# Kernel tuning notes

Measured on AMD Instinct MI355X. Metric: run time of the kernel, lower is better.

The kernel has to match this reference:

```python
import jax, jax.numpy as jnp
import numpy as np

D_MODEL = 1024
NHEADS = 16
E_HEAD = D_MODEL // NHEADS  # 64
ROPE_BASE = 10000.0


def _rope_cos_sin(L, dim, base, dtype):
    # dim = E_head (even); inv_freq over pairs, GPT-NeoX half-split convention
    inv_freq = 1.0 / (base ** (jnp.arange(0, dim, 2, dtype=jnp.float32) / dim))
    pos = jnp.arange(L, dtype=jnp.float32)
    freqs = pos[:, None] * inv_freq[None, :]  # [L, dim/2]
    return jnp.cos(freqs).astype(dtype), jnp.sin(freqs).astype(dtype)


def _apply_rope(t, cos, sin):
    # t: [B, H, L, Dh]; rotate-half formulation
    d2 = t.shape[-1] // 2
    t1, t2 = t[..., :d2], t[..., d2:]
    return jnp.concatenate([t1 * cos - t2 * sin, t1 * sin + t2 * cos], axis=-1)


def setup_inputs() -> dict:
    key = jax.random.key(0)
    ks = jax.random.split(key, 5)
    B, L = 4, 2048
    x = jax.random.normal(ks[0], (B, L, D_MODEL), dtype=jnp.float32)
    s_in = 1.0 / np.sqrt(D_MODEL)
    W_packed = jax.random.normal(ks[1], (3 * D_MODEL, D_MODEL), dtype=jnp.float32) * s_in
    b_packed = jax.random.normal(ks[2], (3 * D_MODEL,), dtype=jnp.float32) * 0.02
    W_out = jax.random.normal(ks[3], (D_MODEL, D_MODEL), dtype=jnp.float32) * s_in
    b_out = jax.random.normal(ks[4], (D_MODEL,), dtype=jnp.float32) * 0.02
    return {"x": x, "W_packed": W_packed, "b_packed": b_packed, "W_out": W_out, "b_out": b_out}


def reference(x, W_packed, b_packed, W_out, b_out):
    B, L, _ = x.shape
    # 1) packed QKV projection (query is key is value path)
    qkv = jnp.einsum('ble,fe->blf', x, W_packed) + b_packed  # [B, L, 3*D]
    q, k, v = jnp.split(qkv, 3, axis=-1)
    # 2) split heads -> [B, H, L, Dh]
    def heads(t):
        return t.reshape(B, L, NHEADS, E_HEAD).transpose(0, 2, 1, 3)
    q, k, v = heads(q), heads(k), heads(v)
    # 3) RoPE on q, k
    cos, sin = _rope_cos_sin(L, E_HEAD, ROPE_BASE, x.dtype)
    q = _apply_rope(q, cos, sin)
    k = _apply_rope(k, cos, sin)
    # 4) SDPA (non-causal, no dropout)
    scale = 1.0 / np.sqrt(E_HEAD)
    scores = jnp.einsum('bhqd,bhkd->bhqk', q, k) * scale
    attn = jax.nn.softmax(scores, axis=-1)
    out = jnp.einsum('bhqk,bhkd->bhqd', attn, v)
    # 5) merge heads + output projection
    out = out.transpose(0, 2, 1, 3).reshape(B, L, D_MODEL)
    return jnp.einsum('bld,ed->ble', out, W_out) + b_out
```

## Files before the change

### kernel.cpp

```cpp
#include <hip/hip_runtime.h>
#include <hip/hip_bf16.h>
#include <stdint.h>

#define L_SEQ 2048
#define NB    4
#define NH    16
#define EH    64
#define DM    1024
#define MTOT  (NB * L_SEQ)

typedef __attribute__((ext_vector_type(8))) short bf16x8;
typedef __attribute__((ext_vector_type(4))) float f32x4;
typedef __attribute__((ext_vector_type(16))) float f32x16;

static __device__ __forceinline__ float bf2f(short u) {
    union { unsigned int i; float f; } c;
    c.i = ((unsigned int)(unsigned short)u) << 16;
    return c.f;
}
static __device__ __forceinline__ short f2bf(float f) {
    union { float f; unsigned int i; } c; c.f = f;
    unsigned int x = c.i;
    unsigned int r = (x + 0x7fffu + ((x >> 16) & 1u)) >> 16;
    return (short)(unsigned short)r;
}
static __device__ __forceinline__ unsigned cvtpk(float lo, float hi) {
    unsigned r;
    asm volatile("v_cvt_pk_bf16_f32 %0, %1, %2" : "=v"(r) : "v"(lo), "v"(hi));
    return r;
}

static __device__ __forceinline__ void gload_lds16(const void* g, void* lds) {
    __builtin_amdgcn_global_load_lds(
        (const __attribute__((address_space(1))) unsigned int*)g,
        (__attribute__((address_space(3))) unsigned int*)lds, 16, 0, 0);
}

__global__ __launch_bounds__(256) void cvt3_k(const float* __restrict__ x,
                                              const float* __restrict__ wp,
                                              const float* __restrict__ wo,
                                              short* __restrict__ xb,
                                              short* __restrict__ wpb,
                                              short* __restrict__ wob,
                                              float* __restrict__ tab) {
    int bid = blockIdx.x;
    if (bid >= 12288) {
        int i = (bid - 12288) * 256 + threadIdx.x;
        int l = i >> 5, d = i & 31;
        float inv = powf(10000.0f, -(float)d * (1.0f / 32.0f));
        float fr = (float)l * inv;
        tab[i]         = cosf(fr);
        tab[65536 + i] = sinf(fr);
        return;
    }
    const float* src; short* dst; int i;
    if (bid < 8192)       { src = x;  dst = xb;  i = bid * 256 + threadIdx.x; }
    else if (bid < 11264) { src = wp; dst = wpb; i = (bid - 8192) * 256 + threadIdx.x; }
    else                  { src = wo; dst = wob; i = (bid - 11264) * 256 + threadIdx.x; }
    float4 v = ((const float4*)src)[i];
    short4 o;
    o.x = f2bf(v.x); o.y = f2bf(v.y); o.z = f2bf(v.z); o.w = f2bf(v.w);
    ((short4*)dst)[i] = o;
}

template<int OUTBF16, int NBN, int NCOL>
__global__ __launch_bounds__(512, 2) void gemmA_k(const short* __restrict__ A,
                                                  const short* __restrict__ Bt,
                                                  const float* __restrict__ bias,
                                                  void* __restrict__ Cv) {
    __shared__ short lds[2][384 * 32];
    const int t = threadIdx.x;
    const int w = t >> 6, l = t & 63;
    const int wm = w >> 1, wn = w & 1;
    const int lr = l & 15, lh = l >> 4;

    const int nblk = NBN * 32;
    int fid = blockIdx.x + blockIdx.y * NBN;
    int swz = (fid & 7) * (nblk >> 3) + (fid >> 3);
    const int n0 = (swz % NBN) * 128;
    const int m0 = (swz / NBN) * 256;

    const int lrow = l >> 2;
    const int schunk = (l & 3) ^ ((l >> 3) & 3);

    const short* Ag = A + (size_t)(m0 + lrow) * 1024 + schunk * 8;
    const short* Bg = Bt + (size_t)(n0 + lrow) * 1024 + schunk * 8;

    auto STAGE = [&](int kt, int buf) {
        gload_lds16(Ag + (size_t)(w * 32) * 1024 + kt * 32,      &lds[buf][(w * 32) * 32]);
        gload_lds16(Ag + (size_t)(w * 32 + 16) * 1024 + kt * 32, &lds[buf][(w * 32 + 16) * 32]);
        gload_lds16(Bg + (size_t)(w * 16) * 1024 + kt * 32,      &lds[buf][8192 + (w * 16) * 32]);
    };

    f32x4 acc[4][4] = {};

    STAGE(0, 0);
    STAGE(1, 1);
    asm volatile("s_waitcnt vmcnt(3)" ::: "memory");
    __builtin_amdgcn_s_barrier();

    const int fch = (lh ^ ((lr >> 1) & 3)) << 3;

#pragma unroll 2
    for (int kt = 0; kt < 32; ++kt) {
        const int c = kt & 1;
        const short* Al = &lds[c][0];
        const short* Bl = &lds[c][8192];

        bf16x8 bfr[4], af[4];
#pragma unroll
        for (int nj = 0; nj < 4; ++nj)
            bfr[nj] = *(const bf16x8*)(Bl + (wn * 64 + nj * 16 + lr) * 32 + fch);
#pragma unroll
        for (int mi = 0; mi < 4; ++mi)
            af[mi] = *(const bf16x8*)(Al + (wm * 64 + mi * 16 + lr) * 32 + fch);

        __builtin_amdgcn_s_setprio(1);
#pragma unroll
        for (int mi = 0; mi < 4; ++mi)
#pragma unroll
            for (int nj = 0; nj < 4; ++nj)
                acc[mi][nj] = __builtin_amdgcn_mfma_f32_16x16x32_bf16(
                    af[mi], bfr[nj], acc[mi][nj], 0, 0, 0);
        __builtin_amdgcn_s_setprio(0);

        asm volatile("s_waitcnt lgkmcnt(0)" ::: "memory");
        __builtin_amdgcn_s_barrier();
        if (kt + 2 < 32) {
            STAGE(kt + 2, c);
            asm volatile("s_waitcnt vmcnt(3)" ::: "memory");
        } else {
            asm volatile("s_waitcnt vmcnt(0)" ::: "memory");
        }
        __builtin_amdgcn_s_barrier();
    }

#pragma unroll
    for (int mi = 0; mi < 4; ++mi) {
#pragma unroll
        for (int nj = 0; nj < 4; ++nj) {
            const int row = m0 + wm * 64 + mi * 16 + lh * 4;
            const int col = n0 + wn * 64 + nj * 16 + lr;
            const float bsv = bias[col];
#pragma unroll
            for (int j = 0; j < 4; ++j) {
                float v = acc[mi][nj][j] + bsv;
                if (OUTBF16)
                    ((short*)Cv)[(size_t)(row + j) * NCOL + col] = f2bf(v);
                else
                    ((float*)Cv)[(size_t)(row + j) * NCOL + col] = v;
            }
        }
    }
}

__global__ __launch_bounds__(256) void gemm_out_k(const short* __restrict__ A,
                                                  const short* __restrict__ Bt,
                                                  const float* __restrict__ bias,
                                                  float* __restrict__ Cv,
                                                  int N, int K) {
    __shared__ short As[128 * 64];
    __shared__ short Bs[128 * 64];
    const int t = threadIdx.x;
    const int w = t >> 6, l = t & 63;
    const int wr = w >> 1, wc = w & 1;
    const int lr = l & 15, lh = l >> 4;
    const int m0 = blockIdx.y * 128, n0 = blockIdx.x * 128;
    const int srow = t >> 3;
    const int scol = (t & 7) * 8;

    f32x4 acc[4][4] = {};

    const short* Ab = A + (size_t)(m0 + srow) * K + scol;
    const short* Bb = Bt + (size_t)(n0 + srow) * K + scol;

    for (int k0 = 0; k0 < K; k0 += 64) {
        __syncthreads();
#pragma unroll
        for (int i = 0; i < 4; i++) {
            gload_lds16(Ab + (size_t)(i * 32) * K + k0, As + i * 2048 + w * 512);
            gload_lds16(Bb + (size_t)(i * 32) * K + k0, Bs + i * 2048 + w * 512);
        }
        __syncthreads();
#pragma unroll
        for (int kk = 0; kk < 2; kk++) {
            bf16x8 af[4], bfr[4];
#pragma unroll
            for (int mi = 0; mi < 4; mi++)
                af[mi] = *(const bf16x8*)(As + (wr * 64 + mi * 16 + lr) * 64 + kk * 32 + lh * 8);
#pragma unroll
            for (int nj = 0; nj < 4; nj++)
                bfr[nj] = *(const bf16x8*)(Bs + (wc * 64 + nj * 16 + lr) * 64 + kk * 32 + lh * 8);
            __builtin_amdgcn_s_setprio(1);
#pragma unroll
            for (int mi = 0; mi < 4; mi++)
#pragma unroll
                for (int nj = 0; nj < 4; nj++)
                    acc[mi][nj] = __builtin_amdgcn_mfma_f32_16x16x32_bf16(
                        af[mi], bfr[nj], acc[mi][nj], 0, 0, 0);
            __builtin_amdgcn_s_setprio(0);
        }
    }
#pragma unroll
    for (int mi = 0; mi < 4; mi++) {
#pragma unroll
        for (int nj = 0; nj < 4; nj++) {
            const int row = m0 + wr * 64 + mi * 16 + lh * 4;
            const int col = n0 + wc * 64 + nj * 16 + lr;
            const float bsv = bias[col];
#pragma unroll
            for (int j = 0; j < 4; j++)
                Cv[(size_t)(row + j) * N + col] = acc[mi][nj][j] + bsv;
        }
    }
}

__global__ __launch_bounds__(256) void scatter_k(const short* __restrict__ qkv,
                                                 const float* __restrict__ tab,
                                                 short* __restrict__ Kd,
                                                 short* __restrict__ Vt) {
    int bid = blockIdx.x;
    if (bid < 4096) {
        int idx = bid * 256 + threadIdx.x;
        int dp = (idx & 7) * 4;
        int h = (idx >> 3) & 15;
        int bl = idx >> 7;
        int l = bl & (L_SEQ - 1);
        int b = bl >> 11;
        float4 cs = *(const float4*)&tab[l * 32 + dp];
        float4 sn = *(const float4*)&tab[65536 + l * 32 + dp];
        const short* row = qkv + (size_t)bl * 3072;
        short4 k1 = *(const short4*)&row[1024 + h * 64 + dp];
        short4 k2 = *(const short4*)&row[1024 + h * 64 + dp + 32];
        size_t ob = ((size_t)((b * 16 + h) * 2048 + l)) * 64;
        union { unsigned u[2]; short4 s4; } e1, e2;
        e1.u[0] = cvtpk(bf2f(k1.x) * cs.x - bf2f(k2.x) * sn.x,
                        bf2f(k1.y) * cs.y - bf2f(k2.y) * sn.y);
        e1.u[1] = cvtpk(bf2f(k1.z) * cs.z - bf2f(k2.z) * sn.z,
                        bf2f(k1.w) * cs.w - bf2f(k2.w) * sn.w);
        e2.u[0] = cvtpk(bf2f(k1.x) * sn.x + bf2f(k2.x) * cs.x,
                        bf2f(k1.y) * sn.y + bf2f(k2.y) * cs.y);
        e2.u[1] = cvtpk(bf2f(k1.z) * sn.z + bf2f(k2.z) * cs.z,
                        bf2f(k1.w) * sn.w + bf2f(k2.w) * cs.w);
        int r7 = l & 7;
        int c1 = ((dp >> 3) ^ r7) * 8 + (dp & 7);
        int c2 = (((dp >> 3) | 4) ^ r7) * 8 + (dp & 7);
        *(short4*)(Kd + ob + c1) = e1.s4;
        *(short4*)(Kd + ob + c2) = e2.s4;
        return;
    }
    __shared__ short tile[64 * 65];
    int bid2 = bid - 4096;
    int l0 = (bid2 & 31) * 64;
    int bh = bid2 >> 5;
    int t = threadIdx.x;
    int b = bh >> 4, h = bh & 15;
#pragma unroll
    for (int i = 0; i < 16; i++) {
        int l = i * 4 + (t >> 6);
        int d = t & 63;
        tile[d * 65 + l] = qkv[(size_t)(b * 2048 + l0 + l) * 3072 + 2048 + h * 64 + d];
    }
    __syncthreads();
#pragma unroll
    for (int i = 0; i < 16; i++) {
        int d = i * 4 + (t >> 6);
        int lx = t & 63;
        int cl = (lx & ~0xC) | ((lx & 4) << 1) | ((lx & 8) >> 1);
        int lp = l0 | ((((cl >> 3) ^ (d & 7)) << 3)) | (cl & 7);
        Vt[(size_t)(bh * 64 + d) * 2048 + lp] = tile[d * 65 + lx];
    }
}

__global__ __launch_bounds__(512, 2) void attn_k(const short* __restrict__ qkv,
                                                 const short* __restrict__ Kg,
                                                 const short* __restrict__ Vt,
                                                 const float* __restrict__ tab,
                                                 short* __restrict__ O) {
    __shared__ short Ks[3][64 * 64];
    __shared__ short Vs[3][64 * 64];
    const int t = threadIdx.x;
    const int w = t >> 6, l = t & 63;
    const int q = l & 31, hi = l >> 5;
    const int r7 = l & 7;

    const int od = blockIdx.x + blockIdx.y * 8;
    const int qblk = (od >> 3) & 7;
    const int bh = (od & 7) * 8 + (od >> 6);
    const int q0 = qblk * 256;
    const int b = bh >> 4, h = bh & 15;

    const short* Kb = Kg + (size_t)bh * (2048 * 64);
    const short* Vb = Vt + (size_t)bh * (64 * 2048);

    const int qrow = q0 + w * 32 + q;

    const short* Qsrc = qkv + (size_t)(b * 2048 + qrow) * 3072 + h * 64;
    bf16x8 qraw[4];
#pragma unroll
    for (int ds = 0; ds < 4; ds++)
        qraw[ds] = *(const bf16x8*)(Qsrc + ds * 16 + hi * 8);
    const float sc = 0.18033688011112042f;
    bf16x8 qf[4];
#pragma unroll
    for (int dsL = 0; dsL < 2; dsL++) {
        bf16x8 r1 = qraw[dsL], r2 = qraw[dsL + 2];
        union { unsigned u[4]; bf16x8 v; } lo, hg;
#pragma unroll
        for (int p = 0; p < 4; p++) {
            float2 c2 = *(const float2*)&tab[qrow * 32 + dsL * 16 + hi * 8 + 2 * p];
            float2 s2 = *(const float2*)&tab[65536 + qrow * 32 + dsL * 16 + hi * 8 + 2 * p];
            float a0 = bf2f(r1[2 * p]),     b0 = bf2f(r2[2 * p]);
            float a1 = bf2f(r1[2 * p + 1]), b1 = bf2f(r2[2 * p + 1]);
            lo.u[p] = cvtpk((a0 * c2.x - b0 * s2.x) * sc, (a1 * c2.y - b1 * s2.y) * sc);
            hg.u[p] = cvtpk((a0 * s2.x + b0 * c2.x) * sc, (a1 * s2.y + b1 * c2.y) * sc);
        }
        qf[dsL] = lo.v; qf[dsL + 2] = hg.v;
    }

    const short one_bf = (short)0x3F80;
    const bf16x8 ones = {one_bf, one_bf, one_bf, one_bf, one_bf, one_bf, one_bf, one_bf};

    f32x16 o0 = {}, o1 = {}, os = {};

    const int grow = w * 8 + (l >> 3);
    const int gcol = r7 * 8;

    gload_lds16(Kb + (size_t)grow * 64 + gcol,        &Ks[0][w * 512]);
    gload_lds16(Vb + (size_t)grow * 2048 + gcol,      &Vs[0][w * 512]);
    gload_lds16(Kb + (size_t)(64 + grow) * 64 + gcol, &Ks[1][w * 512]);
    gload_lds16(Vb + (size_t)grow * 2048 + 64 + gcol, &Vs[1][w * 512]);
    asm volatile("s_waitcnt vmcnt(2)" ::: "memory");
    __builtin_amdgcn_s_barrier();

    const short* Kc = &Ks[0][0];  const short* Vc = &Vs[0][0];
    const short* Kn = &Ks[1][0];  const short* Vn = &Vs[1][0];
    short*       Kf = &Ks[2][0];  short*       Vf = &Vs[2][0];

    for (int it = 0; it < 32; ++it) {
        if (it < 30) {
            const int kn = (it + 2) * 64;
            gload_lds16(Kb + (size_t)(kn + grow) * 64 + gcol, Kf + w * 512);
            gload_lds16(Vb + (size_t)grow * 2048 + kn + gcol, Vf + w * 512);
        }

        f32x16 s0 = {}, s1 = {};
#pragma unroll
        for (int ds = 0; ds < 4; ds++) {
            const int ch = ((ds << 1) | hi) ^ r7;
            bf16x8 k0f = *(const bf16x8*)(Kc + q * 64 + ch * 8);
            bf16x8 k1f = *(const bf16x8*)(Kc + (32 + q) * 64 + ch * 8);
            __builtin_amdgcn_s_setprio(1);
            s0 = __builtin_amdgcn_mfma_f32_32x32x16_bf16(k0f, qf[ds], s0, 0, 0, 0);
            s1 = __builtin_amdgcn_mfma_f32_32x32x16_bf16(k1f, qf[ds], s1, 0, 0, 0);
            __builtin_amdgcn_s_setprio(0);
        }

#pragma unroll
        for (int r = 0; r < 16; r++) {
            s0[r] = __builtin_amdgcn_exp2f(s0[r]);
            s1[r] = __builtin_amdgcn_exp2f(s1[r]);
        }

        bf16x8 pf[4];
        {
            union { unsigned u[4]; bf16x8 v; } f;
            f.u[0] = cvtpk(s0[0], s0[1]);  f.u[1] = cvtpk(s0[2], s0[3]);
            f.u[2] = cvtpk(s0[4], s0[5]);  f.u[3] = cvtpk(s0[6], s0[7]);
            pf[0] = f.v;
            f.u[0] = cvtpk(s0[8], s0[9]);  f.u[1] = cvtpk(s0[10], s0[11]);
            f.u[2] = cvtpk(s0[12], s0[13]); f.u[3] = cvtpk(s0[14], s0[15]);
            pf[1] = f.v;
            f.u[0] = cvtpk(s1[0], s1[1]);  f.u[1] = cvtpk(s1[2], s1[3]);
            f.u[2] = cvtpk(s1[4], s1[5]);  f.u[3] = cvtpk(s1[6], s1[7]);
            pf[2] = f.v;
            f.u[0] = cvtpk(s1[8], s1[9]);  f.u[1] = cvtpk(s1[10], s1[11]);
            f.u[2] = cvtpk(s1[12], s1[13]); f.u[3] = cvtpk(s1[14], s1[15]);
            pf[3] = f.v;
        }

#pragma unroll
        for (int ks = 0; ks < 4; ks++) {
            const int ch = ((ks << 1) | hi) ^ r7;
            bf16x8 v0f = *(const bf16x8*)(Vc + q * 64 + ch * 8);
            bf16x8 v1f = *(const bf16x8*)(Vc + (32 + q) * 64 + ch * 8);
            __builtin_amdgcn_s_setprio(1);
            o0 = __builtin_amdgcn_mfma_f32_32x32x16_bf16(v0f, pf[ks], o0, 0, 0, 0);
            o1 = __builtin_amdgcn_mfma_f32_32x32x16_bf16(v1f, pf[ks], o1, 0, 0, 0);
            os = __builtin_amdgcn_mfma_f32_32x32x16_bf16(ones, pf[ks], os, 0, 0, 0);
            __builtin_amdgcn_s_setprio(0);
        }

        asm volatile("s_waitcnt lgkmcnt(0)" ::: "memory");
        if (it < 30) asm volatile("s_waitcnt vmcnt(2)" ::: "memory");
        else         asm volatile("s_waitcnt vmcnt(0)" ::: "memory");
        __builtin_amdgcn_s_barrier();

        const short* tk = Kc; Kc = Kn; Kn = Kf; Kf = (short*)tk;
        const short* tv = Vc; Vc = Vn; Vn = Vf; Vf = (short*)tv;
    }

    const float inv = 1.0f / os[0];
    short* Orow = O + (size_t)(b * 2048 + qrow) * 1024 + h * 64;
#pragma unroll
    for (int g = 0; g < 4; g++) {
        unsigned w0 = cvtpk(o0[g * 4 + 0] * inv, o0[g * 4 + 1] * inv);
        unsigned w1 = cvtpk(o0[g * 4 + 2] * inv, o0[g * 4 + 3] * inv);
        unsigned long long p0 = (unsigned long long)w0 | ((unsigned long long)w1 << 32);
        *(unsigned long long*)(Orow + g * 8 + hi * 4) = p0;
        unsigned w2 = cvtpk(o1[g * 4 + 0] * inv, o1[g * 4 + 1] * inv);
        unsigned w3 = cvtpk(o1[g * 4 + 2] * inv, o1[g * 4 + 3] * inv);
        unsigned long long p1 = (unsigned long long)w2 | ((unsigned long long)w3 << 32);
        *(unsigned long long*)(Orow + 32 + g * 8 + hi * 4) = p1;
    }
}

extern "C" void kernel_launch(void* const* d_in, const int* in_sizes, int n_in,
                              void* d_out, int out_size, void* d_ws, size_t ws_size,
                              hipStream_t stream) {
    const float* x  = (const float*)d_in[0];
    const float* Wp = (const float*)d_in[1];
    const float* bp = (const float*)d_in[2];
    const float* Wo = (const float*)d_in[3];
    const float* bo = (const float*)d_in[4];

    char* ws = (char*)d_ws;
    const size_t SZ_XB  = (size_t)MTOT * DM * 2;
    const size_t SZ_WPB = (size_t)3 * DM * DM * 2;
    const size_t SZ_WOB = (size_t)DM * DM * 2;
    const size_t SZ_QKV = (size_t)MTOT * 3 * DM * 2;
    const size_t SZ_BHLE = (size_t)MTOT * DM * 2;

    short* xb   = (short*)(ws);
    short* wpb  = (short*)(ws + SZ_XB);
    short* wob  = (short*)(ws + SZ_XB + SZ_WPB);
    short* qkvb = (short*)(ws + SZ_XB + SZ_WPB + SZ_WOB);
    short* Kb   = (short*)(ws + SZ_XB + SZ_WPB + SZ_WOB + SZ_QKV);
    short* Vtb  = (short*)(ws + SZ_XB + SZ_WPB + SZ_WOB + SZ_QKV + SZ_BHLE);
    short* Ob   = (short*)(ws + SZ_XB + SZ_WPB + SZ_WOB + SZ_QKV + 2 * SZ_BHLE);
    float* tab  = (float*)(ws + SZ_XB + SZ_WPB + SZ_WOB + SZ_QKV + 3 * SZ_BHLE);

    cvt3_k<<<12544, 256, 0, stream>>>(x, Wp, Wo, xb, wpb, wob, tab);

    gemmA_k<1, 24, 3072><<<dim3(24, 32), 512, 0, stream>>>(xb, wpb, bp, qkvb);

    scatter_k<<<6144, 256, 0, stream>>>(qkvb, tab, Kb, Vtb);

    attn_k<<<dim3(8, 64), 512, 0, stream>>>(qkvb, Kb, Vtb, tab, Ob);

    gemm_out_k<<<dim3(8, 64), 256, 0, stream>>>(Ob, wob, bo, (float*)d_out, DM, DM);
}
```

Baseline: 198.9 us.

## Precompute scaled RoPE Q in scatter kernel; reuse gemmA for output projection

Moves the RoPE rotation and softmax scaling of Q from the attention kernel into the scatter kernel, which now writes a contiguous per-head Q buffer. The attention prologue becomes plain vector loads instead of strided qkv reads plus table lookups. The separate 256-thread output GEMM is dropped and the templated 512-thread gemmA kernel is reused with fp32 output (128x... tiles, 8x32 grid). This costs an extra Q write and read through global memory, and the output GEMM grid shrinks from 512 to 256 blocks.

```diff
diff --git a/kernel.cpp b/kernel.cpp
--- a/kernel.cpp
+++ b/kernel.cpp
@@ -154,69 +154,9 @@
     }
 }
 
-__global__ __launch_bounds__(256) void gemm_out_k(const short* __restrict__ A,
-                                                  const short* __restrict__ Bt,
-                                                  const float* __restrict__ bias,
-                                                  float* __restrict__ Cv,
-                                                  int N, int K) {
-    __shared__ short As[128 * 64];
-    __shared__ short Bs[128 * 64];
-    const int t = threadIdx.x;
-    const int w = t >> 6, l = t & 63;
-    const int wr = w >> 1, wc = w & 1;
-    const int lr = l & 15, lh = l >> 4;
-    const int m0 = blockIdx.y * 128, n0 = blockIdx.x * 128;
-    const int srow = t >> 3;
-    const int scol = (t & 7) * 8;
-
-    f32x4 acc[4][4] = {};
-
-    const short* Ab = A + (size_t)(m0 + srow) * K + scol;
-    const short* Bb = Bt + (size_t)(n0 + srow) * K + scol;
-
-    for (int k0 = 0; k0 < K; k0 += 64) {
-        __syncthreads();
-#pragma unroll
-        for (int i = 0; i < 4; i++) {
-            gload_lds16(Ab + (size_t)(i * 32) * K + k0, As + i * 2048 + w * 512);
-            gload_lds16(Bb + (size_t)(i * 32) * K + k0, Bs + i * 2048 + w * 512);
-        }
-        __syncthreads();
-#pragma unroll
-        for (int kk = 0; kk < 2; kk++) {
-            bf16x8 af[4], bfr[4];
-#pragma unroll
-            for (int mi = 0; mi < 4; mi++)
-                af[mi] = *(const bf16x8*)(As + (wr * 64 + mi * 16 + lr) * 64 + kk * 32 + lh * 8);
-#pragma unroll
-            for (int nj = 0; nj < 4; nj++)
-                bfr[nj] = *(const bf16x8*)(Bs + (wc * 64 + nj * 16 + lr) * 64 + kk * 32 + lh * 8);
-            __builtin_amdgcn_s_setprio(1);
-#pragma unroll
-            for (int mi = 0; mi < 4; mi++)
-#pragma unroll
-                for (int nj = 0; nj < 4; nj++)
-                    acc[mi][nj] = __builtin_amdgcn_mfma_f32_16x16x32_bf16(
-                        af[mi], bfr[nj], acc[mi][nj], 0, 0, 0);
-            __builtin_amdgcn_s_setprio(0);
-        }
-    }
-#pragma unroll
-    for (int mi = 0; mi < 4; mi++) {
-#pragma unroll
-        for (int nj = 0; nj < 4; nj++) {
-            const int row = m0 + wr * 64 + mi * 16 + lh * 4;
-            const int col = n0 + wc * 64 + nj * 16 + lr;
-            const float bsv = bias[col];
-#pragma unroll
-            for (int j = 0; j < 4; j++)
-                Cv[(size_t)(row + j) * N + col] = acc[mi][nj][j] + bsv;
-        }
-    }
-}
-
 __global__ __launch_bounds__(256) void scatter_k(const short* __restrict__ qkv,
                                                  const float* __restrict__ tab,
+                                                 short* __restrict__ Q,
                                                  short* __restrict__ Kd,
                                                  short* __restrict__ Vt) {
     int bid = blockIdx.x;
@@ -230,9 +170,23 @@
         float4 cs = *(const float4*)&tab[l * 32 + dp];
         float4 sn = *(const float4*)&tab[65536 + l * 32 + dp];
         const short* row = qkv + (size_t)bl * 3072;
+        size_t ob = ((size_t)((b * 16 + h) * 2048 + l)) * 64;
+        const float sc = 0.18033688011112042f;
+        short4 q1 = *(const short4*)&row[h * 64 + dp];
+        short4 q2 = *(const short4*)&row[h * 64 + dp + 32];
+        union { unsigned u[2]; short4 s4; } a1, a2;
+        a1.u[0] = cvtpk((bf2f(q1.x) * cs.x - bf2f(q2.x) * sn.x) * sc,
+                        (bf2f(q1.y) * cs.y - bf2f(q2.y) * sn.y) * sc);
+        a1.u[1] = cvtpk((bf2f(q1.z) * cs.z - bf2f(q2.z) * sn.z) * sc,
+                        (bf2f(q1.w) * cs.w - bf2f(q2.w) * sn.w) * sc);
+        a2.u[0] = cvtpk((bf2f(q1.x) * sn.x + bf2f(q2.x) * cs.x) * sc,
+                        (bf2f(q1.y) * sn.y + bf2f(q2.y) * cs.y) * sc);
+        a2.u[1] = cvtpk((bf2f(q1.z) * sn.z + bf2f(q2.z) * cs.z) * sc,
+                        (bf2f(q1.w) * sn.w + bf2f(q2.w) * cs.w) * sc);
+        *(short4*)(Q + ob + dp)      = a1.s4;
+        *(short4*)(Q + ob + dp + 32) = a2.s4;
         short4 k1 = *(const short4*)&row[1024 + h * 64 + dp];
         short4 k2 = *(const short4*)&row[1024 + h * 64 + dp + 32];
-        size_t ob = ((size_t)((b * 16 + h) * 2048 + l)) * 64;
         union { unsigned u[2]; short4 s4; } e1, e2;
         e1.u[0] = cvtpk(bf2f(k1.x) * cs.x - bf2f(k2.x) * sn.x,
                         bf2f(k1.y) * cs.y - bf2f(k2.y) * sn.y);
@@ -272,10 +226,9 @@
     }
 }
 
-__global__ __launch_bounds__(512, 2) void attn_k(const short* __restrict__ qkv,
+__global__ __launch_bounds__(512, 2) void attn_k(const short* __restrict__ Qg,
                                                  const short* __restrict__ Kg,
                                                  const short* __restrict__ Vt,
-                                                 const float* __restrict__ tab,
                                                  short* __restrict__ O) {
     __shared__ short Ks[3][64 * 64];
     __shared__ short Vs[3][64 * 64];
@@ -288,35 +241,16 @@
     const int qblk = (od >> 3) & 7;
     const int bh = (od & 7) * 8 + (od >> 6);
     const int q0 = qblk * 256;
-    const int b = bh >> 4, h = bh & 15;
-
+
+    const short* Qb = Qg + (size_t)bh * (2048 * 64);
     const short* Kb = Kg + (size_t)bh * (2048 * 64);
     const short* Vb = Vt + (size_t)bh * (64 * 2048);
 
     const int qrow = q0 + w * 32 + q;
-
-    const short* Qsrc = qkv + (size_t)(b * 2048 + qrow) * 3072 + h * 64;
-    bf16x8 qraw[4];
+    bf16x8 qf[4];
 #pragma unroll
     for (int ds = 0; ds < 4; ds++)
-        qraw[ds] = *(const bf16x8*)(Qsrc + ds * 16 + hi * 8);
-    const float sc = 0.18033688011112042f;
-    bf16x8 qf[4];
-#pragma unroll
-    for (int dsL = 0; dsL < 2; dsL++) {
-        bf16x8 r1 = qraw[dsL], r2 = qraw[dsL + 2];
-        union { unsigned u[4]; bf16x8 v; } lo, hg;
-#pragma unroll
-        for (int p = 0; p < 4; p++) {
-            float2 c2 = *(const float2*)&tab[qrow * 32 + dsL * 16 + hi * 8 + 2 * p];
-            float2 s2 = *(const float2*)&tab[65536 + qrow * 32 + dsL * 16 + hi * 8 + 2 * p];
-            float a0 = bf2f(r1[2 * p]),     b0 = bf2f(r2[2 * p]);
-            float a1 = bf2f(r1[2 * p + 1]), b1 = bf2f(r2[2 * p + 1]);
-            lo.u[p] = cvtpk((a0 * c2.x - b0 * s2.x) * sc, (a1 * c2.y - b1 * s2.y) * sc);
-            hg.u[p] = cvtpk((a0 * s2.x + b0 * c2.x) * sc, (a1 * s2.y + b1 * c2.y) * sc);
-        }
-        qf[dsL] = lo.v; qf[dsL + 2] = hg.v;
-    }
+        qf[ds] = *(const bf16x8*)(Qb + (size_t)qrow * 64 + ds * 16 + hi * 8);
 
     const short one_bf = (short)0x3F80;
     const bf16x8 ones = {one_bf, one_bf, one_bf, one_bf, one_bf, one_bf, one_bf, one_bf};
@@ -401,6 +335,7 @@
     }
 
     const float inv = 1.0f / os[0];
+    const int b = bh >> 4, h = bh & 15;
     short* Orow = O + (size_t)(b * 2048 + qrow) * 1024 + h * 64;
 #pragma unroll
     for (int g = 0; g < 4; g++) {
@@ -435,18 +370,19 @@
     short* wpb  = (short*)(ws + SZ_XB);
     short* wob  = (short*)(ws + SZ_XB + SZ_WPB);
     short* qkvb = (short*)(ws + SZ_XB + SZ_WPB + SZ_WOB);
-    short* Kb   = (short*)(ws + SZ_XB + SZ_WPB + SZ_WOB + SZ_QKV);
-    short* Vtb  = (short*)(ws + SZ_XB + SZ_WPB + SZ_WOB + SZ_QKV + SZ_BHLE);
-    short* Ob   = (short*)(ws + SZ_XB + SZ_WPB + SZ_WOB + SZ_QKV + 2 * SZ_BHLE);
-    float* tab  = (float*)(ws + SZ_XB + SZ_WPB + SZ_WOB + SZ_QKV + 3 * SZ_BHLE);
+    short* Qb   = (short*)(ws + SZ_XB + SZ_WPB + SZ_WOB + SZ_QKV);
+    short* Kb   = (short*)(ws + SZ_XB + SZ_WPB + SZ_WOB + SZ_QKV + SZ_BHLE);
+    short* Vtb  = (short*)(ws + SZ_XB + SZ_WPB + SZ_WOB + SZ_QKV + 2 * SZ_BHLE);
+    short* Ob   = (short*)(ws + SZ_XB + SZ_WPB + SZ_WOB + SZ_QKV + 3 * SZ_BHLE);
+    float* tab  = (float*)(ws + SZ_XB + SZ_WPB + SZ_WOB + SZ_QKV + 4 * SZ_BHLE);
 
     cvt3_k<<<12544, 256, 0, stream>>>(x, Wp, Wo, xb, wpb, wob, tab);
 
     gemmA_k<1, 24, 3072><<<dim3(24, 32), 512, 0, stream>>>(xb, wpb, bp, qkvb);
 
-    scatter_k<<<6144, 256, 0, stream>>>(qkvb, tab, Kb, Vtb);
-
-    attn_k<<<dim3(8, 64), 512, 0, stream>>>(qkvb, Kb, Vtb, tab, Ob);
-
-    gemm_out_k<<<dim3(8, 64), 256, 0, stream>>>(Ob, wob, bo, (float*)d_out, DM, DM);
-}
+    scatter_k<<<6144, 256, 0, stream>>>(qkvb, tab, Qb, Kb, Vtb);
+
+    attn_k<<<dim3(8, 64), 512, 0, stream>>>(Qb, Kb, Vtb, Ob);
+
+    gemmA_k<0, 8, 1024><<<dim3(8, 32), 512, 0, stream>>>(Ob, wob, bo, (float*)d_out);
+}
```

After: 191.4 us. 1.04x faster.
